# Optimization experiments

Measured on AMD Instinct MI355X. Metric: run time of the kernel, lower is better.

The kernel has to match this reference:

```python
import jax, jax.numpy as jnp
import numpy as np
from math import pi

K = 3        # kernel_size
STRIDE = 1
PADDING = 1


def _ringify(v):
    # wrap to (-pi, pi], matching torch's (x + pi) % (2*pi) - pi
    return (v + pi) % (2.0 * pi) - pi


def setup_inputs() -> dict:
    key = jax.random.key(0)
    kx, kw = jax.random.split(key)
    x = jax.random.normal(kx, (4, 16, 64, 64), dtype=jnp.float32)
    # torch: Parameter(empty(1, C_in, C_out, 1, 1, k, k).uniform_(-pi, pi))
    weight = jax.random.uniform(kw, (1, 16, 32, 1, 1, K, K),
                                minval=-pi, maxval=pi, dtype=jnp.float32)
    return {"x": x, "weight": weight}


def reference(x, weight):
    # zero-pad spatial dims (constant 0, like F.pad mode='constant')
    xp = jnp.pad(x, ((0, 0), (0, 0), (PADDING, PADDING), (PADDING, PADDING)))
    B, C, H, W = xp.shape
    Ho = (H - K) // STRIDE + 1
    Wo = (W - K) // STRIDE + 1
    # unfold: patches[b, c, ho, wo, kh, kw] == xp[b, c, ho*s + kh, wo*s + kw]
    patches = jnp.stack(
        [jnp.stack([xp[:, :, i:i + Ho * STRIDE:STRIDE, j:j + Wo * STRIDE:STRIDE]
                    for j in range(K)], axis=-1)
         for i in range(K)], axis=-2)              # (B, C_in, Ho, Wo, kH, kW)
    # broadcast against weight (1, C_in, C_out, 1, 1, kH, kW)
    diff = _ringify(patches[:, :, None] - weight)  # (B, C_in, C_out, Ho, Wo, kH, kW)
    # circular mean over (C_in, kH, kW): angle of summed unit vectors
    dir_x = jnp.cos(diff).sum(axis=(1, 5, 6))      # (B, C_out, Ho, Wo)
    dir_y = jnp.sin(diff).sum(axis=(1, 5, 6))
    return jnp.arctan2(dir_y, dir_x)
```

## Files before the change

kernel.cpp:

```cpp
#include <hip/hip_runtime.h>
#include <math.h>

#define CI 16
#define CO 32
#define HH 64
#define WW 64
#define KK 3
#define TH 4
#define TW 16
#define HALO_H (TH + 2)
#define HALO_W (TW + 2)


__global__ __launch_bounds__(256)
void RingConv2dSimple_kernel(const float* __restrict__ x,
                             const float* __restrict__ w,
                             float* __restrict__ out) {
    __shared__ float2 wcs[CI * CO * 9];
    __shared__ float2 xs[CI][HALO_H][HALO_W];

    const int tid = threadIdx.x;
    const int b   = blockIdx.z;
    const int th0 = blockIdx.y * TH;
    const int tw0 = blockIdx.x * TW;

    for (int i = tid; i < CI * CO * 9; i += 256) {
        float wv = w[i];
        float s, c;
        __sincosf(wv, &s, &c);
        wcs[i] = make_float2(c, s);
    }

    for (int i = tid; i < CI * HALO_H * HALO_W; i += 256) {
        int ci  = i / (HALO_H * HALO_W);
        int rem = i - ci * (HALO_H * HALO_W);
        int r   = rem / HALO_W;
        int c   = rem - r * HALO_W;
        int h  = th0 + r - 1;
        int ww = tw0 + c - 1;
        float xv = 0.0f;
        if (h >= 0 && h < HH && ww >= 0 && ww < WW)
            xv = x[((b * CI + ci) * HH + h) * WW + ww];
        float s, c2;
        __sincosf(xv, &s, &c2);
        xs[ci][r][c] = make_float2(c2, s);
    }
    __syncthreads();

    const int lane = tid & 63;
    const int wid  = tid >> 6;
    const int r    = lane >> 4;
    const int c    = lane & 15;

    float ax[8], ay[8];
    #pragma unroll
    for (int j = 0; j < 8; ++j) { ax[j] = 0.0f; ay[j] = 0.0f; }

    for (int ci = 0; ci < CI; ++ci) {
        #pragma unroll
        for (int kh = 0; kh < KK; ++kh) {
            #pragma unroll
            for (int kw = 0; kw < KK; ++kw) {
                const float2 p = xs[ci][r + kh][c + kw];
                const float2* wrow = &wcs[(ci * CO + wid * 8) * 9 + kh * 3 + kw];
                #pragma unroll
                for (int j = 0; j < 8; ++j) {
                    const float2 wv = wrow[j * 9];
                    ax[j] = fmaf(p.x, wv.x, fmaf(p.y, wv.y, ax[j]));
                    ay[j] = fmaf(p.y, wv.x, fmaf(-p.x, wv.y, ay[j]));
                }
            }
        }
    }

    #pragma unroll
    for (int j = 0; j < 8; ++j) {
        const int co = wid * 8 + j;
        out[((b * CO + co) * HH + (th0 + r)) * WW + (tw0 + c)] =
            atan2f(ay[j], ax[j]);
    }
}

extern "C" void kernel_launch(void* const* d_in, const int* in_sizes, int n_in,
                              void* d_out, int out_size, void* d_ws, size_t ws_size,
                              hipStream_t stream) {
    const float* x = (const float*)d_in[0];
    const float* w = (const float*)d_in[1];
    float* out = (float*)d_out;

    const int B = in_sizes[0] / (CI * HH * WW);
    dim3 grid(WW / TW, HH / TH, B);
    RingConv2dSimple_kernel<<<grid, 256, 0, stream>>>(x, w, out);
}
```

Measured before the change: 19.47 us.

## Precompute weight sincos in a prep kernel and split output channels across 16 waves

Adds a separate kernel that computes cos/sin of the weights once into a workspace table, laid out so each output-channel pair's taps sit contiguously. The main kernel drops the per-block weight sincos and its large shared-memory table. It reads weights from global memory at wave-uniform addresses, which allows scalar loads via readfirstlane. Blocks grow to 1024 threads, each wave handling two output channels instead of eight, which cuts accumulator registers and raises parallelism. In exchange it adds a second launch and spreads the halo sincos work over more threads.

```diff
diff --git a/kernel.cpp b/kernel.cpp
--- a/kernel.cpp
+++ b/kernel.cpp
@@ -10,13 +10,29 @@
 #define TW 16
 #define HALO_H (TH + 2)
 #define HALO_W (TW + 2)
+#define NTAP 9
 
 
 __global__ __launch_bounds__(256)
-void RingConv2dSimple_kernel(const float* __restrict__ x,
-                             const float* __restrict__ w,
-                             float* __restrict__ out) {
-    __shared__ float2 wcs[CI * CO * 9];
+void ringconv_wprep(const float* __restrict__ w, float* __restrict__ wtab) {
+    int i = blockIdx.x * 256 + threadIdx.x;
+    if (i >= CI * CO * NTAP) return;
+    int ci  = i / (CO * NTAP);
+    int rem = i - ci * (CO * NTAP);
+    int co  = rem / NTAP;
+    int tap = rem - co * NTAP;
+    float s, c;
+    __sincosf(w[i], &s, &c);
+    int cg = co >> 1, col = co & 1;
+    float* dst = wtab + (((cg * CI + ci) * NTAP + tap) << 2) + (col << 1);
+    dst[0] = c;
+    dst[1] = s;
+}
+
+__global__ __launch_bounds__(1024)
+void ringconv_main(const float* __restrict__ x,
+                   const float* __restrict__ wtab,
+                   float* __restrict__ out) {
     __shared__ float2 xs[CI][HALO_H][HALO_W];
 
     const int tid = threadIdx.x;
@@ -24,37 +40,31 @@
     const int th0 = blockIdx.y * TH;
     const int tw0 = blockIdx.x * TW;
 
-    for (int i = tid; i < CI * CO * 9; i += 256) {
-        float wv = w[i];
-        float s, c;
-        __sincosf(wv, &s, &c);
-        wcs[i] = make_float2(c, s);
-    }
-
-    for (int i = tid; i < CI * HALO_H * HALO_W; i += 256) {
+    for (int i = tid; i < CI * HALO_H * HALO_W; i += 1024) {
         int ci  = i / (HALO_H * HALO_W);
         int rem = i - ci * (HALO_H * HALO_W);
-        int r   = rem / HALO_W;
-        int c   = rem - r * HALO_W;
-        int h  = th0 + r - 1;
-        int ww = tw0 + c - 1;
+        int rr  = rem / HALO_W;
+        int cc  = rem - rr * HALO_W;
+        int h  = th0 + rr - 1;
+        int ww = tw0 + cc - 1;
         float xv = 0.0f;
         if (h >= 0 && h < HH && ww >= 0 && ww < WW)
             xv = x[((b * CI + ci) * HH + h) * WW + ww];
         float s, c2;
         __sincosf(xv, &s, &c2);
-        xs[ci][r][c] = make_float2(c2, s);
+        xs[ci][rr][cc] = make_float2(c2, s);
     }
     __syncthreads();
 
     const int lane = tid & 63;
     const int wid  = tid >> 6;
+    const int cg   = __builtin_amdgcn_readfirstlane(wid);
     const int r    = lane >> 4;
     const int c    = lane & 15;
 
-    float ax[8], ay[8];
-    #pragma unroll
-    for (int j = 0; j < 8; ++j) { ax[j] = 0.0f; ay[j] = 0.0f; }
+    const float* __restrict__ wt = wtab + cg * (CI * NTAP * 4);
+
+    float ax0 = 0.f, ay0 = 0.f, ax1 = 0.f, ay1 = 0.f;
 
     for (int ci = 0; ci < CI; ++ci) {
         #pragma unroll
@@ -62,23 +72,21 @@
             #pragma unroll
             for (int kw = 0; kw < KK; ++kw) {
                 const float2 p = xs[ci][r + kh][c + kw];
-                const float2* wrow = &wcs[(ci * CO + wid * 8) * 9 + kh * 3 + kw];
-                #pragma unroll
-                for (int j = 0; j < 8; ++j) {
-                    const float2 wv = wrow[j * 9];
-                    ax[j] = fmaf(p.x, wv.x, fmaf(p.y, wv.y, ax[j]));
-                    ay[j] = fmaf(p.y, wv.x, fmaf(-p.x, wv.y, ay[j]));
-                }
+                const float* w4 = wt + ((ci * NTAP + kh * KK + kw) << 2);
+                const float wc0 = w4[0], ws0 = w4[1];
+                const float wc1 = w4[2], ws1 = w4[3];
+                ax0 = fmaf(p.x, wc0, fmaf(p.y,  ws0, ax0));
+                ay0 = fmaf(p.y, wc0, fmaf(p.x, -ws0, ay0));
+                ax1 = fmaf(p.x, wc1, fmaf(p.y,  ws1, ax1));
+                ay1 = fmaf(p.y, wc1, fmaf(p.x, -ws1, ay1));
             }
         }
     }
 
-    #pragma unroll
-    for (int j = 0; j < 8; ++j) {
-        const int co = wid * 8 + j;
-        out[((b * CO + co) * HH + (th0 + r)) * WW + (tw0 + c)] =
-            atan2f(ay[j], ax[j]);
-    }
+    const int co0 = cg * 2;
+    const int oidx = ((b * CO + co0) * HH + (th0 + r)) * WW + (tw0 + c);
+    out[oidx]           = atan2f(ay0, ax0);
+    out[oidx + HH * WW] = atan2f(ay1, ax1);
 }
 
 extern "C" void kernel_launch(void* const* d_in, const int* in_sizes, int n_in,
@@ -86,9 +94,13 @@
                               hipStream_t stream) {
     const float* x = (const float*)d_in[0];
     const float* w = (const float*)d_in[1];
-    float* out = (float*)d_out;
+    float* out  = (float*)d_out;
+    float* wtab = (float*)d_ws;
 
     const int B = in_sizes[0] / (CI * HH * WW);
+
+    ringconv_wprep<<<(CI * CO * NTAP + 255) / 256, 256, 0, stream>>>(w, wtab);
+
     dim3 grid(WW / TW, HH / TH, B);
-    RingConv2dSimple_kernel<<<grid, 256, 0, stream>>>(x, w, out);
+    ringconv_main<<<grid, 1024, 0, stream>>>(x, wtab, out);
 }
```

New measurement: 18.92 us. 1.03x faster.
